# Kernel optimization log

Measured on AMD Instinct MI355X. Metric: run time of the kernel, lower is better.

## Reference

```python
import jax, jax.numpy as jnp
import numpy as np

NUM_EMBEDDINGS = 8192
EMBEDDING_DIM = 256
COMMITMENT_COST = 0.25
DECAY = 0.99
EPS = 1e-05


def setup_inputs() -> dict:
    key = jax.random.key(0)
    k1, k2, k3 = jax.random.split(key, 3)
    x = jax.random.normal(k1, (16, 256, 32, 32), dtype=jnp.float32)
    emb = jax.random.normal(k2, (NUM_EMBEDDINGS, EMBEDDING_DIM), dtype=jnp.float32) * 0.1
    emb = emb / jnp.linalg.norm(emb, axis=1, keepdims=True)  # F.normalize(dim=1)
    return {
        "x": x,
        "embedding": emb,
        "cluster_size": jnp.ones((NUM_EMBEDDINGS,), dtype=jnp.float32),
        "embed_avg": emb,
    }


def reference(x, embedding, cluster_size, embed_avg):
    K, D = embedding.shape
    n = x.ndim
    # permute channels (dim 1) to last, flatten to [N, D]
    perm_fwd = (0,) + tuple(range(2, n)) + (1,)
    px = jnp.transpose(x, perm_fwd)
    flat = px.reshape(-1, D)  # [N, D]

    # squared L2 distances (monotone in cdist p=2) -> argmin nearest code
    d = (
        jnp.sum(flat * flat, axis=1, keepdims=True)
        - 2.0 * (flat @ embedding.T)
        + jnp.sum(embedding * embedding, axis=1)
    )  # [N, K]
    idx = jnp.argmin(d, axis=1)  # [N]

    # gather-by-index instead of one-hot @ embedding (same math)
    quantized = embedding[idx].reshape(px.shape)
    perm_back = (0, n - 1) + tuple(range(1, n - 1))
    quantized = jnp.transpose(quantized, perm_back)  # back to x layout

    # EMA buffer updates (training path, no_grad in torch)
    counts = jax.ops.segment_sum(
        jnp.ones_like(idx, dtype=flat.dtype), idx, num_segments=K
    )  # == encodings.sum(0)
    new_cluster_size = cluster_size * DECAY + (1.0 - DECAY) * counts
    dw = jax.ops.segment_sum(flat, idx, num_segments=K)  # == encodings.T @ flat
    new_embed_avg = embed_avg * DECAY + (1.0 - DECAY) * dw
    new_embedding = new_embed_avg / jnp.maximum(new_cluster_size, EPS)[:, None]

    # commitment loss (quantized detached)
    loss = COMMITMENT_COST * jnp.mean((x - jax.lax.stop_gradient(quantized)) ** 2)

    # straight-through estimator
    quantized_st = x + jax.lax.stop_gradient(quantized - x)

    avg_probs = counts / flat.shape[0]  # == encodings.mean(0)
    perplexity = jnp.exp(-jnp.sum(avg_probs * jnp.log(avg_probs + 1e-10)))

    return (quantized_st, loss, perplexity, new_embedding, new_cluster_size, new_embed_avg)
```

## Files before the change

kernel.cpp:

```cpp
#include <hip/hip_runtime.h>
#include <stdint.h>

#define K_CODES 8192
#define D 256
#define NROWS 16384
#define NELEM 4194304

#define WS_ENORM   0x00000u
#define WS_KEYS    0x08000u
#define WS_ICOUNTS 0x28000u
#define WS_CURSOR  0x30000u
#define WS_BASE    0x38000u
#define WS_ROWLIST 0x40000u
#define WS_PART    0x50000u
#define WS_XHI     0x60000u
#define WS_XLO     (WS_XHI + 0x800000u)
#define WS_EHI     (WS_XLO + 0x800000u)
#define WS_ELO     (WS_EHI + 0x400000u)

#define O_QST  0
#define O_LOSS 4194304
#define O_PERP 4194305
#define O_EMB  4194306
#define O_CS   6291458
#define O_EAVG 6299650

typedef unsigned short u16;
typedef __attribute__((ext_vector_type(8))) short bf16x8;
typedef __attribute__((ext_vector_type(4))) float f32x4;

__device__ __forceinline__ u16 f2bf(float f) {
    uint32_t u = __float_as_uint(f);
    u += 0x7FFFu + ((u >> 16) & 1u);
    return (u16)(u >> 16);
}
__device__ __forceinline__ float bf2f(u16 h) {
    return __uint_as_float(((uint32_t)h) << 16);
}

__device__ __forceinline__ void glds16(const u16* g, u16* lds_base) {
    __builtin_amdgcn_global_load_lds(
        (const __attribute__((address_space(1))) uint32_t*)g,
        (__attribute__((address_space(3))) uint32_t*)lds_base, 16, 0, 0);
}

__global__ __launch_bounds__(256) void prep_kernel(const float* __restrict__ emb,
                                                   const float* __restrict__ x,
                                                   u16* __restrict__ eh,
                                                   u16* __restrict__ el,
                                                   float* __restrict__ enorm,
                                                   u16* __restrict__ xhi,
                                                   u16* __restrict__ xlo,
                                                   unsigned long long* __restrict__ keys,
                                                   int* __restrict__ icounts,
                                                   int* __restrict__ cursor) {
    __shared__ u16 Lh[64][72];
    __shared__ u16 Ll[64][72];
    const int bid = blockIdx.x, t = threadIdx.x;
    if (bid < 8192) {
        const int k = bid;
        const size_t i = (size_t)k * D + t;
        const float v = emb[i];
        const u16 h = f2bf(v);
        eh[i] = h;
        el[i] = f2bf(v - bf2f(h));
        float s = v * v;
#pragma unroll
        for (int off = 32; off; off >>= 1) s += __shfl_down(s, off, 64);
        __shared__ float sm[4];
        if ((t & 63) == 0) sm[t >> 6] = s;
        __syncthreads();
        if (t == 0) enorm[k] = sm[0] + sm[1] + sm[2] + sm[3];
    } else if (bid < 9216) {
        const int px = bid - 8192;
        const int hw0 = (px & 15) << 6;
        const int c0 = ((px >> 4) & 3) << 6;
        const int b = px >> 6;
        const int l = t & 63, w = t >> 6;
#pragma unroll
        for (int i = 0; i < 16; ++i) {
            const int cl = w * 16 + i;
            const float v = x[(((size_t)(b * 256 + c0 + cl)) << 10) + hw0 + l];
            const u16 h = f2bf(v);
            Lh[l][cl] = h;
            Ll[l][cl] = f2bf(v - bf2f(h));
        }
        __syncthreads();
        const int r = t >> 2, cs = t & 3;
        const size_t n = (((size_t)b) << 10) + hw0 + r;
        const size_t o = n * D + c0 + cs * 16;
        *(uint4*)&xhi[o]     = *(const uint4*)&Lh[r][cs * 16];
        *(uint4*)&xhi[o + 8] = *(const uint4*)&Lh[r][cs * 16 + 8];
        *(uint4*)&xlo[o]     = *(const uint4*)&Ll[r][cs * 16];
        *(uint4*)&xlo[o + 8] = *(const uint4*)&Ll[r][cs * 16 + 8];
    } else {
        const int n = (bid - 9216) * 256 + t;
        keys[n] = ~0ull;
        if (n < K_CODES) { icounts[n] = 0; cursor[n] = 0; }
    }
}

#define BM 128
#define BN 128
#define SLICES 2
#define CT_PER 32

__global__ __launch_bounds__(256, 1) void dist_kernel(const u16* __restrict__ xhi,
                                                      const u16* __restrict__ xlo,
                                                      const u16* __restrict__ ehi,
                                                      const u16* __restrict__ elo,
                                                      const float* __restrict__ enorm,
                                                      unsigned long long* __restrict__ keys) {
    extern __shared__ __align__(16) u16 lds[];

    const int tid = threadIdx.x;
    const int l = tid & 63, w = tid >> 6;
    const int wr = w >> 1, wc = w & 1;
    const int slice = blockIdx.x;
    const int n0 = blockIdx.y * BM;
    const int md = l & 15, quad = l >> 4;

#pragma unroll
    for (int wd = 0; wd < 16; ++wd) {
        const int win = w * 16 + wd;
        const int rA = 2 * win + (l >> 5);
        const int g = (l & 31) ^ (rA & 31);
        const size_t src = (size_t)(n0 + rA) * D + g * 8;
        glds16(xhi + src, &lds[win * 512]);
        glds16(xlo + src, &lds[32768 + win * 512]);
    }

    int rbase[4], rh[4];
#pragma unroll
    for (int i = 0; i < 4; ++i) {
        const int rA = wr * 64 + i * 16 + md;
        rbase[i] = rA * 256;
        rh[i] = rA & 31;
    }

    __syncthreads();

    bf16x8 falo[8][4];
#pragma unroll
    for (int kt = 0; kt < 8; ++kt)
#pragma unroll
        for (int i = 0; i < 4; ++i) {
            const int slot = ((kt << 2) | quad) ^ rh[i];
            falo[kt][i] = *(const bf16x8*)&lds[32768 + rbase[i] + slot * 8];
        }

    __syncthreads();

    const int WB = 32768 + w * 8192;
    const int rloc = l >> 3, sB = l & 7, gB = sB ^ rloc;
    const u16* PB[8];
#pragma unroll
    for (int c8 = 0; c8 < 8; ++c8) {
        const u16* pl = (gB & 4) ? elo : ehi;
        PB[c8] = pl + (size_t)(slice * 4096 + wc * 64 + c8 * 8 + rloc) * D + (gB & 3) * 8;
    }
#pragma unroll
    for (int c8 = 0; c8 < 8; ++c8) glds16(PB[c8], &lds[WB + c8 * 512]);

    int offBH[4], offBL[4];
#pragma unroll
    for (int j = 0; j < 4; ++j) {
        const int cloc = j * 16 + md;
        offBH[j] = WB + cloc * 64 + ((quad) ^ (md & 7)) * 8;
        offBL[j] = WB + cloc * 64 + ((quad + 4) ^ (md & 7)) * 8;
    }

    float rbv[4][4];
    int rbi[4][4];
#pragma unroll
    for (int i = 0; i < 4; ++i)
#pragma unroll
        for (int r = 0; r < 4; ++r) { rbv[i][r] = 1e30f; rbi[i][r] = 0; }

    f32x4 acc[4][4];
#pragma unroll
    for (int i = 0; i < 4; ++i)
#pragma unroll
        for (int j = 0; j < 4; ++j) acc[i][j] = (f32x4)0.f;

    bf16x8 fahi[2][4], fbh[2][4], fbl[2][4];

    float ecr[4];
#pragma unroll
    for (int j = 0; j < 4; ++j) ecr[j] = enorm[slice * 4096 + wc * 64 + j * 16 + md];

    for (int ct = 0; ct < CT_PER; ++ct) {
#pragma unroll
        for (int kt = 0; kt < 8; ++kt) {
            __builtin_amdgcn_s_waitcnt(0x0F70);
            __builtin_amdgcn_sched_barrier(0);
            const int m = ct * 8 + kt;
            if (m < CT_PER * 8 - 1) {
                const int m1 = m + 1;
                const int soff = (m1 >> 3) * 32768 + (m1 & 7) * 32;
                const int db = WB + ((m1 & 1) << 12);
#pragma unroll
                for (int c8 = 0; c8 < 8; ++c8) glds16(PB[c8] + soff, &lds[db + c8 * 512]);
            }
            const int p = kt & 1, bufo = p << 12;
#pragma unroll
            for (int i = 0; i < 4; ++i) {
                const int slot = ((kt << 2) | quad) ^ rh[i];
                fahi[p][i] = *(const bf16x8*)&lds[rbase[i] + slot * 8];
            }
#pragma unroll
            for (int j = 0; j < 4; ++j) {
                fbh[p][j] = *(const bf16x8*)&lds[bufo + offBH[j]];
                fbl[p][j] = *(const bf16x8*)&lds[bufo + offBL[j]];
            }
            if (kt > 0 || ct > 0) {
                const int q = p ^ 1;
                const int kq = (kt + 7) & 7;
#pragma unroll
                for (int i = 0; i < 4; ++i)
#pragma unroll
                    for (int j = 0; j < 4; ++j) {
                        acc[i][j] = __builtin_amdgcn_mfma_f32_16x16x32_bf16(fahi[q][i], fbh[q][j], acc[i][j], 0, 0, 0);
                        acc[i][j] = __builtin_amdgcn_mfma_f32_16x16x32_bf16(fahi[q][i], fbl[q][j], acc[i][j], 0, 0, 0);
                        acc[i][j] = __builtin_amdgcn_mfma_f32_16x16x32_bf16(falo[kq][i], fbh[q][j], acc[i][j], 0, 0, 0);
                    }
                if (kt == 0) {
                    const int gc0 = slice * 4096 + (ct - 1) * 128;
#pragma unroll
                    for (int i = 0; i < 4; ++i)
#pragma unroll
                        for (int r = 0; r < 4; ++r)
#pragma unroll
                            for (int j = 0; j < 4; ++j) {
                                const float s = fmaf(-2.f, acc[i][j][r], ecr[j]);
                                const int ci = gc0 + wc * 64 + j * 16 + md;
                                if (s < rbv[i][r]) { rbv[i][r] = s; rbi[i][r] = ci; }
                            }
#pragma unroll
                    for (int j = 0; j < 4; ++j)
                        ecr[j] = enorm[slice * 4096 + ct * 128 + wc * 64 + j * 16 + md];
#pragma unroll
                    for (int i = 0; i < 4; ++i)
#pragma unroll
                        for (int j = 0; j < 4; ++j) acc[i][j] = (f32x4)0.f;
                }
            }
        }
    }

    {
#pragma unroll
        for (int i = 0; i < 4; ++i)
#pragma unroll
            for (int j = 0; j < 4; ++j) {
                acc[i][j] = __builtin_amdgcn_mfma_f32_16x16x32_bf16(fahi[1][i], fbh[1][j], acc[i][j], 0, 0, 0);
                acc[i][j] = __builtin_amdgcn_mfma_f32_16x16x32_bf16(fahi[1][i], fbl[1][j], acc[i][j], 0, 0, 0);
                acc[i][j] = __builtin_amdgcn_mfma_f32_16x16x32_bf16(falo[7][i], fbh[1][j], acc[i][j], 0, 0, 0);
            }
        const int gc0 = slice * 4096 + (CT_PER - 1) * 128;
#pragma unroll
        for (int i = 0; i < 4; ++i)
#pragma unroll
            for (int r = 0; r < 4; ++r)
#pragma unroll
                for (int j = 0; j < 4; ++j) {
                    const float s = fmaf(-2.f, acc[i][j][r], ecr[j]);
                    const int ci = gc0 + wc * 64 + j * 16 + md;
                    if (s < rbv[i][r]) { rbv[i][r] = s; rbi[i][r] = ci; }
                }
    }

#pragma unroll
    for (int i = 0; i < 4; ++i)
#pragma unroll
        for (int r = 0; r < 4; ++r) {
            float bv = rbv[i][r];
            int bi = rbi[i][r];
#pragma unroll
            for (int m = 1; m < 16; m <<= 1) {
                const float ov = __shfl_xor(bv, m, 64);
                const int oi = __shfl_xor(bi, m, 64);
                if (ov < bv || (ov == bv && oi < bi)) { bv = ov; bi = oi; }
            }
            if (md == 0) {
                unsigned int u = __float_as_uint(bv);
                u = (u & 0x80000000u) ? ~u : (u | 0x80000000u);
                const unsigned long long key = ((unsigned long long)u << 32) | (unsigned int)bi;
                atomicMin(&keys[n0 + wr * 64 + i * 16 + quad * 4 + r], key);
            }
        }
}

__global__ __launch_bounds__(256) void quant_loss_kernel(const float* __restrict__ x,
                                                         const float* __restrict__ emb,
                                                         const unsigned long long* __restrict__ keys,
                                                         float* __restrict__ out,
                                                         float* __restrict__ partials,
                                                         int* __restrict__ icounts) {
    const int blk = blockIdx.x;
    const int b = blk >> 4;
    const int hw0 = (blk & 15) << 6;
    const int l = threadIdx.x & 63;
    const int cq = threadIdx.x >> 6;
    const int hw = hw0 + l;
    const int n = (b << 10) + hw;
    const int code = (int)(keys[n] & 0xFFFFFFFFull);
    if (threadIdx.x < 64) atomicAdd(&icounts[code], 1);
    const float* erow = emb + (size_t)code * D;
    const float* xb = x + (((size_t)b * 256) << 10) + hw;
    float* ob = out + O_QST + (((size_t)b * 256) << 10) + hw;
    float lsum = 0.f;
#pragma unroll 4
    for (int c = cq; c < D; c += 4) {
        const float xv = xb[(size_t)c << 10];
        const float ev = erow[c];
        ob[(size_t)c << 10] = xv + (ev - xv);
        const float d = xv - ev;
        lsum = fmaf(d, d, lsum);
    }
    __shared__ float sm[4];
    const int lane = threadIdx.x & 63, wv = threadIdx.x >> 6;
#pragma unroll
    for (int off = 32; off; off >>= 1) lsum += __shfl_down(lsum, off, 64);
    if (lane == 0) sm[wv] = lsum;
    __syncthreads();
    if (threadIdx.x == 0) partials[blockIdx.x] = sm[0] + sm[1] + sm[2] + sm[3];
}

__global__ __launch_bounds__(256) void scan_final_kernel(const int* __restrict__ icounts,
                                                         int* __restrict__ basearr,
                                                         const float* __restrict__ partials,
                                                         float* __restrict__ out) {
    const int t = threadIdx.x, lane = t & 63, w = t >> 6;
    int loc = 0;
    float ps = 0.f;
    for (int i = 0; i < 32; ++i) {
        const int c = icounts[t * 32 + i];
        loc += c;
        const float p = (float)c * (1.0f / 16384.0f);
        ps += p * logf(p + 1e-10f);
    }
    int v = loc;
#pragma unroll
    for (int off = 1; off < 64; off <<= 1) {
        const int u = __shfl_up(v, off, 64);
        if (lane >= off) v += u;
    }
    __shared__ int wsum[4];
    __shared__ float fs[8];
    if (lane == 63) wsum[w] = v;
    float lp = partials[t];
#pragma unroll
    for (int off = 32; off; off >>= 1) {
        lp += __shfl_down(lp, off, 64);
        ps += __shfl_down(ps, off, 64);
    }
    if (lane == 0) { fs[w] = lp; fs[4 + w] = ps; }
    __syncthreads();
    int pre = 0;
    for (int i = 0; i < w; ++i) pre += wsum[i];
    int b = pre + v - loc;
    for (int i = 0; i < 32; ++i) {
        basearr[t * 32 + i] = b;
        b += icounts[t * 32 + i];
    }
    if (t == 0) {
        out[O_LOSS] = 0.25f * ((fs[0] + fs[1] + fs[2] + fs[3]) / 4194304.0f);
        out[O_PERP] = expf(-(fs[4] + fs[5] + fs[6] + fs[7]));
    }
}

__global__ __launch_bounds__(256) void slot_kernel(const unsigned long long* __restrict__ keys,
                                                   const int* __restrict__ basearr,
                                                   int* __restrict__ cursor,
                                                   int* __restrict__ rowlist) {
    const int n = blockIdx.x * 256 + threadIdx.x;
    const int code = (int)(keys[n] & 0xFFFFFFFFull);
    const int pos = atomicAdd(&cursor[code], 1);
    rowlist[basearr[code] + pos] = n;
}

__global__ __launch_bounds__(256) void gather_ema_kernel(const u16* __restrict__ xhi,
                                                         const u16* __restrict__ xlo,
                                                         const int* __restrict__ icounts,
                                                         const int* __restrict__ basearr,
                                                         const int* __restrict__ rowlist,
                                                         const float* __restrict__ embed_avg,
                                                         const float* __restrict__ cluster_size,
                                                         float* __restrict__ out) {
    const int k = blockIdx.x, c = threadIdx.x;
    const int cnt = icounts[k], b0 = basearr[k];
    float s = 0.f;
    for (int t = 0; t < cnt; ++t) {
        const int n = rowlist[b0 + t];
        s += bf2f(xhi[(size_t)n * D + c]) + bf2f(xlo[(size_t)n * D + c]);
    }
    const float ncs = cluster_size[k] * 0.99f + 0.01f * (float)cnt;
    const size_t i = (size_t)k * D + c;
    const float na = embed_avg[i] * 0.99f + 0.01f * s;
    out[O_EAVG + i] = na;
    out[O_EMB + i] = na / fmaxf(ncs, 1e-5f);
    if (c == 0) out[O_CS + k] = ncs;
}

extern "C" void kernel_launch(void* const* d_in, const int* in_sizes, int n_in,
                              void* d_out, int out_size, void* d_ws, size_t ws_size,
                              hipStream_t stream) {
    const float* x            = (const float*)d_in[0];
    const float* emb          = (const float*)d_in[1];
    const float* cluster_size = (const float*)d_in[2];
    const float* embed_avg    = (const float*)d_in[3];
    float* out = (float*)d_out;
    char* ws = (char*)d_ws;

    float* enorm = (float*)(ws + WS_ENORM);
    unsigned long long* keys = (unsigned long long*)(ws + WS_KEYS);
    int* icounts = (int*)(ws + WS_ICOUNTS);
    int* cursor = (int*)(ws + WS_CURSOR);
    int* basearr = (int*)(ws + WS_BASE);
    int* rowlist = (int*)(ws + WS_ROWLIST);
    float* partials = (float*)(ws + WS_PART);
    u16* xhi = (u16*)(ws + WS_XHI);
    u16* xlo = (u16*)(ws + WS_XLO);
    u16* ehi = (u16*)(ws + WS_EHI);
    u16* elo = (u16*)(ws + WS_ELO);

    static int lds_attr_set = 0;
    if (!lds_attr_set) {
        hipFuncSetAttribute((const void*)dist_kernel,
                            hipFuncAttributeMaxDynamicSharedMemorySize, 131072);
        lds_attr_set = 1;
    }

    prep_kernel<<<9280, 256, 0, stream>>>(emb, x, ehi, elo, enorm, xhi, xlo,
                                          keys, icounts, cursor);
    dist_kernel<<<dim3(SLICES, NROWS / BM), 256, 131072, stream>>>(xhi, xlo, ehi, elo, enorm, keys);
    quant_loss_kernel<<<256, 256, 0, stream>>>(x, emb, keys, out, partials, icounts);
    scan_final_kernel<<<1, 256, 0, stream>>>(icounts, basearr, partials, out);
    slot_kernel<<<NROWS / 256, 256, 0, stream>>>(keys, basearr, cursor, rowlist);
    gather_ema_kernel<<<K_CODES, 256, 0, stream>>>(xhi, xlo, icounts, basearr, rowlist,
                                                   embed_avg, cluster_size, out);
}
```

Baseline: 293.6 us.

## Halve dist-kernel row tile, share B tile across waves, two blocks per CU

Result: slower. 331.5 us (+12.9%).

```diff
diff --git a/kernel.cpp b/kernel.cpp
--- a/kernel.cpp
+++ b/kernel.cpp
@@ -100,12 +100,12 @@
     }
 }
 
-#define BM 128
+#define BM 64
 #define BN 128
 #define SLICES 2
 #define CT_PER 32
 
-__global__ __launch_bounds__(256, 1) void dist_kernel(const u16* __restrict__ xhi,
+__global__ __launch_bounds__(256, 2) void dist_kernel(const u16* __restrict__ xhi,
                                                       const u16* __restrict__ xlo,
                                                       const u16* __restrict__ ehi,
                                                       const u16* __restrict__ elo,
@@ -115,25 +115,24 @@
 
     const int tid = threadIdx.x;
     const int l = tid & 63, w = tid >> 6;
-    const int wr = w >> 1, wc = w & 1;
     const int slice = blockIdx.x;
     const int n0 = blockIdx.y * BM;
     const int md = l & 15, quad = l >> 4;
 
 #pragma unroll
-    for (int wd = 0; wd < 16; ++wd) {
-        const int win = w * 16 + wd;
+    for (int wd = 0; wd < 8; ++wd) {
+        const int win = w * 8 + wd;
         const int rA = 2 * win + (l >> 5);
         const int g = (l & 31) ^ (rA & 31);
         const size_t src = (size_t)(n0 + rA) * D + g * 8;
         glds16(xhi + src, &lds[win * 512]);
-        glds16(xlo + src, &lds[32768 + win * 512]);
+        glds16(xlo + src, &lds[16384 + win * 512]);
     }
 
     int rbase[4], rh[4];
 #pragma unroll
     for (int i = 0; i < 4; ++i) {
-        const int rA = wr * 64 + i * 16 + md;
+        const int rA = i * 16 + md;
         rbase[i] = rA * 256;
         rh[i] = rA & 31;
     }
@@ -146,28 +145,28 @@
 #pragma unroll
         for (int i = 0; i < 4; ++i) {
             const int slot = ((kt << 2) | quad) ^ rh[i];
-            falo[kt][i] = *(const bf16x8*)&lds[32768 + rbase[i] + slot * 8];
+            falo[kt][i] = *(const bf16x8*)&lds[16384 + rbase[i] + slot * 8];
         }
 
     __syncthreads();
 
-    const int WB = 32768 + w * 8192;
     const int rloc = l >> 3, sB = l & 7, gB = sB ^ rloc;
-    const u16* PB[8];
-#pragma unroll
-    for (int c8 = 0; c8 < 8; ++c8) {
+    const u16* PB[4];
+#pragma unroll
+    for (int c4 = 0; c4 < 4; ++c4) {
         const u16* pl = (gB & 4) ? elo : ehi;
-        PB[c8] = pl + (size_t)(slice * 4096 + wc * 64 + c8 * 8 + rloc) * D + (gB & 3) * 8;
-    }
-#pragma unroll
-    for (int c8 = 0; c8 < 8; ++c8) glds16(PB[c8], &lds[WB + c8 * 512]);
-
-    int offBH[4], offBL[4];
-#pragma unroll
-    for (int j = 0; j < 4; ++j) {
-        const int cloc = j * 16 + md;
-        offBH[j] = WB + cloc * 64 + ((quad) ^ (md & 7)) * 8;
-        offBL[j] = WB + cloc * 64 + ((quad + 4) ^ (md & 7)) * 8;
+        PB[c4] = pl + (size_t)(slice * 4096 + w * 32 + c4 * 8 + rloc) * D + (gB & 3) * 8;
+    }
+#pragma unroll
+    for (int c4 = 0; c4 < 4; ++c4)
+        glds16(PB[c4], &lds[16384 + (w * 4 + c4) * 512]);
+
+    int offBH[2], offBL[2];
+#pragma unroll
+    for (int j = 0; j < 2; ++j) {
+        const int cloc = w * 32 + j * 16 + md;
+        offBH[j] = cloc * 64 + ((quad) ^ (md & 7)) * 8;
+        offBL[j] = cloc * 64 + ((quad + 4) ^ (md & 7)) * 8;
     }
 
     float rbv[4][4];
@@ -177,97 +176,67 @@
 #pragma unroll
         for (int r = 0; r < 4; ++r) { rbv[i][r] = 1e30f; rbi[i][r] = 0; }
 
-    f32x4 acc[4][4];
+    f32x4 acc[4][2];
 #pragma unroll
     for (int i = 0; i < 4; ++i)
 #pragma unroll
-        for (int j = 0; j < 4; ++j) acc[i][j] = (f32x4)0.f;
-
-    bf16x8 fahi[2][4], fbh[2][4], fbl[2][4];
-
-    float ecr[4];
-#pragma unroll
-    for (int j = 0; j < 4; ++j) ecr[j] = enorm[slice * 4096 + wc * 64 + j * 16 + md];
+        for (int j = 0; j < 2; ++j) acc[i][j] = (f32x4)0.f;
 
     for (int ct = 0; ct < CT_PER; ++ct) {
+        float ecr[2];
+#pragma unroll
+        for (int j = 0; j < 2; ++j)
+            ecr[j] = enorm[slice * 4096 + ct * 128 + w * 32 + j * 16 + md];
+
 #pragma unroll
         for (int kt = 0; kt < 8; ++kt) {
-            __builtin_amdgcn_s_waitcnt(0x0F70);
-            __builtin_amdgcn_sched_barrier(0);
+            __syncthreads();
             const int m = ct * 8 + kt;
             if (m < CT_PER * 8 - 1) {
                 const int m1 = m + 1;
                 const int soff = (m1 >> 3) * 32768 + (m1 & 7) * 32;
-                const int db = WB + ((m1 & 1) << 12);
-#pragma unroll
-                for (int c8 = 0; c8 < 8; ++c8) glds16(PB[c8] + soff, &lds[db + c8 * 512]);
+                const int db = 16384 + ((m1 & 1) << 13);
+#pragma unroll
+                for (int c4 = 0; c4 < 4; ++c4)
+                    glds16(PB[c4] + soff, &lds[db + (w * 4 + c4) * 512]);
             }
-            const int p = kt & 1, bufo = p << 12;
+            const int bb = 16384 + ((m & 1) << 13);
+            bf16x8 fahi[4], fbh[2], fbl[2];
 #pragma unroll
             for (int i = 0; i < 4; ++i) {
                 const int slot = ((kt << 2) | quad) ^ rh[i];
-                fahi[p][i] = *(const bf16x8*)&lds[rbase[i] + slot * 8];
+                fahi[i] = *(const bf16x8*)&lds[rbase[i] + slot * 8];
             }
 #pragma unroll
-            for (int j = 0; j < 4; ++j) {
-                fbh[p][j] = *(const bf16x8*)&lds[bufo + offBH[j]];
-                fbl[p][j] = *(const bf16x8*)&lds[bufo + offBL[j]];
+            for (int j = 0; j < 2; ++j) {
+                fbh[j] = *(const bf16x8*)&lds[bb + offBH[j]];
+                fbl[j] = *(const bf16x8*)&lds[bb + offBL[j]];
             }
-            if (kt > 0 || ct > 0) {
-                const int q = p ^ 1;
-                const int kq = (kt + 7) & 7;
-#pragma unroll
-                for (int i = 0; i < 4; ++i)
-#pragma unroll
-                    for (int j = 0; j < 4; ++j) {
-                        acc[i][j] = __builtin_amdgcn_mfma_f32_16x16x32_bf16(fahi[q][i], fbh[q][j], acc[i][j], 0, 0, 0);
-                        acc[i][j] = __builtin_amdgcn_mfma_f32_16x16x32_bf16(fahi[q][i], fbl[q][j], acc[i][j], 0, 0, 0);
-                        acc[i][j] = __builtin_amdgcn_mfma_f32_16x16x32_bf16(falo[kq][i], fbh[q][j], acc[i][j], 0, 0, 0);
-                    }
-                if (kt == 0) {
-                    const int gc0 = slice * 4096 + (ct - 1) * 128;
-#pragma unroll
-                    for (int i = 0; i < 4; ++i)
-#pragma unroll
-                        for (int r = 0; r < 4; ++r)
-#pragma unroll
-                            for (int j = 0; j < 4; ++j) {
-                                const float s = fmaf(-2.f, acc[i][j][r], ecr[j]);
-                                const int ci = gc0 + wc * 64 + j * 16 + md;
-                                if (s < rbv[i][r]) { rbv[i][r] = s; rbi[i][r] = ci; }
-                            }
-#pragma unroll
-                    for (int j = 0; j < 4; ++j)
-                        ecr[j] = enorm[slice * 4096 + ct * 128 + wc * 64 + j * 16 + md];
-#pragma unroll
-                    for (int i = 0; i < 4; ++i)
-#pragma unroll
-                        for (int j = 0; j < 4; ++j) acc[i][j] = (f32x4)0.f;
+#pragma unroll
+            for (int i = 0; i < 4; ++i)
+#pragma unroll
+                for (int j = 0; j < 2; ++j) {
+                    acc[i][j] = __builtin_amdgcn_mfma_f32_16x16x32_bf16(fahi[i],     fbh[j], acc[i][j], 0, 0, 0);
+                    acc[i][j] = __builtin_amdgcn_mfma_f32_16x16x32_bf16(fahi[i],     fbl[j], acc[i][j], 0, 0, 0);
+                    acc[i][j] = __builtin_amdgcn_mfma_f32_16x16x32_bf16(falo[kt][i], fbh[j], acc[i][j], 0, 0, 0);
                 }
-            }
         }
-    }
-
-    {
+
+        const int gc0 = slice * 4096 + ct * 128 + w * 32;
 #pragma unroll
         for (int i = 0; i < 4; ++i)
 #pragma unroll
-            for (int j = 0; j < 4; ++j) {
-                acc[i][j] = __builtin_amdgcn_mfma_f32_16x16x32_bf16(fahi[1][i], fbh[1][j], acc[i][j], 0, 0, 0);
-                acc[i][j] = __builtin_amdgcn_mfma_f32_16x16x32_bf16(fahi[1][i], fbl[1][j], acc[i][j], 0, 0, 0);
-                acc[i][j] = __builtin_amdgcn_mfma_f32_16x16x32_bf16(falo[7][i], fbh[1][j], acc[i][j], 0, 0, 0);
-            }
-        const int gc0 = slice * 4096 + (CT_PER - 1) * 128;
-#pragma unroll
-        for (int i = 0; i < 4; ++i)
-#pragma unroll
             for (int r = 0; r < 4; ++r)
 #pragma unroll
-                for (int j = 0; j < 4; ++j) {
+                for (int j = 0; j < 2; ++j) {
                     const float s = fmaf(-2.f, acc[i][j][r], ecr[j]);
-                    const int ci = gc0 + wc * 64 + j * 16 + md;
+                    const int ci = gc0 + j * 16 + md;
                     if (s < rbv[i][r]) { rbv[i][r] = s; rbi[i][r] = ci; }
                 }
+#pragma unroll
+        for (int i = 0; i < 4; ++i)
+#pragma unroll
+            for (int j = 0; j < 2; ++j) acc[i][j] = (f32x4)0.f;
     }
 
 #pragma unroll
@@ -286,7 +255,7 @@
                 unsigned int u = __float_as_uint(bv);
                 u = (u & 0x80000000u) ? ~u : (u | 0x80000000u);
                 const unsigned long long key = ((unsigned long long)u << 32) | (unsigned int)bi;
-                atomicMin(&keys[n0 + wr * 64 + i * 16 + quad * 4 + r], key);
+                atomicMin(&keys[n0 + i * 16 + quad * 4 + r], key);
             }
         }
 }
@@ -428,13 +397,13 @@
     static int lds_attr_set = 0;
     if (!lds_attr_set) {
         hipFuncSetAttribute((const void*)dist_kernel,
-                            hipFuncAttributeMaxDynamicSharedMemorySize, 131072);
+                            hipFuncAttributeMaxDynamicSharedMemorySize, 65536);
         lds_attr_set = 1;
     }
 
     prep_kernel<<<9280, 256, 0, stream>>>(emb, x, ehi, elo, enorm, xhi, xlo,
                                           keys, icounts, cursor);
-    dist_kernel<<<dim3(SLICES, NROWS / BM), 256, 131072, stream>>>(xhi, xlo, ehi, elo, enorm, keys);
+    dist_kernel<<<dim3(SLICES, NROWS / BM), 256, 65536, stream>>>(xhi, xlo, ehi, elo, enorm, keys);
     quant_loss_kernel<<<256, 256, 0, stream>>>(x, emb, keys, out, partials, icounts);
     scan_final_kernel<<<1, 256, 0, stream>>>(icounts, basearr, partials, out);
     slot_kernel<<<NROWS / 256, 256, 0, stream>>>(keys, basearr, cursor, rowlist);
```
